# Kernel optimization log

Hardware: AMD Instinct MI355X
Metric: run time of the kernel (lower is better)

## Reference

```python
import jax, jax.numpy as jnp
import numpy as np

HEADS = 16

def _rope(x):
    # x: (B, H, T, D); rotate pairs (even, odd) along last dim, positions along axis 2
    B, H, T, D = x.shape
    half = D // 2
    theta = 10000.0 ** (-jnp.arange(half, dtype=x.dtype) / half)          # (half,)
    angles = jnp.arange(T, dtype=x.dtype)[:, None] * theta                # (T, half)
    sin, cos = jnp.sin(angles), jnp.cos(angles)                           # (T, half)
    x1, x2 = x[..., ::2], x[..., 1::2]                                    # (B,H,T,half)
    rot = jnp.stack([x1 * cos - x2 * sin, x1 * sin + x2 * cos], axis=-1)  # (B,H,T,half,2)
    return rot.reshape(B, H, T, D)

def setup_inputs() -> dict:
    key = jax.random.key(0)
    k1, k2, k3 = jax.random.split(key, 3)
    B, T, C = 2, 2048, 1024
    return {
        "x": jax.random.normal(k1, (B, T, C), dtype=jnp.float32),
        "W_qkv": jax.random.normal(k2, (3 * C, C), dtype=jnp.float32) * 0.02,
        "W_out": jax.random.normal(k3, (C, C), dtype=jnp.float32) * 0.02,
        "window": 256,
    }

def reference(x, W_qkv, W_out, window):
    B, T, C = x.shape
    H = HEADS
    D = C // H
    # fused QKV projection (torch Linear: y = x @ W.T)
    qkv = jnp.einsum('btc,fc->btf', x, W_qkv)            # (B,T,3C)
    qkv = qkv.reshape(B, T, H, 3 * D).transpose(0, 2, 1, 3)  # (B,H,T,3D)
    q, k, v = jnp.split(qkv, 3, axis=-1)                 # each (B,H,T,D)
    q, k = _rope(q), _rope(k)
    # causal + local-window boolean mask: allow j in [i-window, i]
    i = jnp.arange(T)[:, None]
    j = jnp.arange(T)[None, :]
    mask = (j <= i) & (j >= i - window)                  # (T,T) bool
    scale = 1.0 / jnp.sqrt(jnp.asarray(D, dtype=x.dtype))
    scores = jnp.einsum('bhqd,bhkd->bhqk', q, k) * scale # (B,H,T,T)
    scores = jnp.where(mask[None, None], scores, -jnp.inf)
    attn = jax.nn.softmax(scores, axis=-1)
    out = jnp.einsum('bhqk,bhkd->bhqd', attn, v)         # (B,H,T,D)
    out = out.transpose(0, 2, 1, 3).reshape(B, T, C)
    return jnp.einsum('btc,oc->bto', out, W_out)
```

## Files before the change

### kernel.cpp

```cpp
#include <hip/hip_runtime.h>

typedef float f32x4 __attribute__((ext_vector_type(4)));
typedef __bf16 bf16x8 __attribute__((ext_vector_type(8)));
typedef unsigned short u16x4 __attribute__((ext_vector_type(4)));

__device__ __forceinline__ unsigned short f2bf(float f) {
  union { float f; unsigned int u; } v; v.f = f;
  unsigned int r = (v.u + 0x7FFFu + ((v.u >> 16) & 1u)) >> 16;
  return (unsigned short)r;
}
__device__ __forceinline__ float bf2f(unsigned short h) {
  union { unsigned int u; float f; } v; v.u = ((unsigned int)h) << 16;
  return v.f;
}
__device__ __forceinline__ void gload_lds16(const void* g, void* l) {
  __builtin_amdgcn_global_load_lds(
      (const __attribute__((address_space(1))) unsigned int*)g,
      (__attribute__((address_space(3))) unsigned int*)l, 16, 0, 0);
}

__global__ __launch_bounds__(256) void prep_kernel(
    const float* __restrict__ x, const float* __restrict__ wqkv,
    const float* __restrict__ wout, unsigned short* __restrict__ xb,
    unsigned short* __restrict__ wqkvb, unsigned short* __restrict__ woutb,
    float2* __restrict__ tab) {
  const int N1 = 1048576, N2 = 786432, N3 = 262144;
  int idx = blockIdx.x * 256 + threadIdx.x;
  if (idx < N1 + N2 + N3) {
    const float* src; unsigned short* dst; int i = idx;
    if (i < N1)           { src = x;    dst = xb; }
    else if (i < N1 + N2) { i -= N1;      src = wqkv; dst = wqkvb; }
    else                  { i -= N1 + N2; src = wout; dst = woutb; }
    float4 v = ((const float4*)src)[i];
    u16x4 o;
    o.x = f2bf(v.x); o.y = f2bf(v.y); o.z = f2bf(v.z); o.w = f2bf(v.w);
    ((u16x4*)dst)[i] = o;
  } else {
    int i = idx - (N1 + N2 + N3);
    if (i < 65536) {
      int t = i >> 5, p = i & 31;
      float theta = exp2f(-(float)p * 0.4152410118609203f);
      float sn, cs;
      sincosf((float)t * theta, &sn, &cs);
      tab[i] = make_float2(cs, sn);
    }
  }
}

template <bool OUTBF16>
__global__ __launch_bounds__(256) void gemm_bt(const unsigned short* __restrict__ A,
                                               const unsigned short* __restrict__ B,
                                               void* __restrict__ C,
                                               int M, int N, int K) {
  __shared__ unsigned short As[128][32];
  __shared__ unsigned short Bs[128][32];
  const int tid = threadIdx.x;
  const int lane = tid & 63;
  const int w = tid >> 6, wr = w >> 1, wc = w & 1;
  const int bm = blockIdx.y * 128, bn = blockIdx.x * 128;
  const int t4 = tid >> 2, c8 = (tid & 3) * 8;
  const unsigned short* Ab = A + (size_t)(bm + t4) * K + c8;
  const unsigned short* Bb = B + (size_t)(bn + t4) * K + c8;
  const int rq = lane & 15, kg = (lane >> 4) * 8;
  f32x4 acc[4][4] = {};
  for (int kt = 0; kt < K; kt += 32) {
    gload_lds16(Ab + kt,                  &As[t4][c8]);
    gload_lds16(Ab + kt + (size_t)64 * K, &As[t4 + 64][c8]);
    gload_lds16(Bb + kt,                  &Bs[t4][c8]);
    gload_lds16(Bb + kt + (size_t)64 * K, &Bs[t4 + 64][c8]);
    __syncthreads();
    bf16x8 fa[4], fb[4];
#pragma unroll
    for (int m = 0; m < 4; ++m) fa[m] = *(const bf16x8*)&As[wr * 64 + m * 16 + rq][kg];
#pragma unroll
    for (int n = 0; n < 4; ++n) fb[n] = *(const bf16x8*)&Bs[wc * 64 + n * 16 + rq][kg];
#pragma unroll
    for (int m = 0; m < 4; ++m)
#pragma unroll
      for (int n = 0; n < 4; ++n)
        acc[m][n] = __builtin_amdgcn_mfma_f32_16x16x32_bf16(fa[m], fb[n], acc[m][n], 0, 0, 0);
    __syncthreads();
  }
  const int r0 = bm + wr * 64 + (lane >> 4) * 4;
  const int c0 = bn + wc * 64 + rq;
#pragma unroll
  for (int m = 0; m < 4; ++m)
#pragma unroll
    for (int n = 0; n < 4; ++n)
#pragma unroll
      for (int j = 0; j < 4; ++j) {
        int row = r0 + m * 16 + j, col = c0 + n * 16;
        if (OUTBF16)
          ((unsigned short*)C)[(size_t)row * N + col] = f2bf(acc[m][n][j]);
        else
          ((float*)C)[(size_t)row * N + col] = acc[m][n][j];
      }
}

#define WMAX 256

__device__ __forceinline__ void rope16(unsigned short* e, const float2* __restrict__ tb) {
#pragma unroll
  for (int p = 0; p < 8; ++p) {
    float2 cs = tb[p];
    float a = bf2f(e[2 * p]), b = bf2f(e[2 * p + 1]);
    e[2 * p]     = f2bf(a * cs.x - b * cs.y);
    e[2 * p + 1] = f2bf(a * cs.y + b * cs.x);
  }
}

__global__ __launch_bounds__(256) void attn_kernel(const unsigned short* __restrict__ qkv,
                                                   unsigned short* __restrict__ attnb,
                                                   const int* __restrict__ winp,
                                                   const float2* __restrict__ tab) {
  __shared__ unsigned short Qs[64][72];
  __shared__ unsigned short KPs[320 * 72];
  __shared__ unsigned short Vt[64][328];
  const int T = 2048;
  const int tid = threadIdx.x;
  const int bid = blockIdx.x;
  const int qt = bid & 31;
  const int bh = bid >> 5;
  const int b = bh >> 4, h = bh & 15;
  const int qbase = qt * 64;
  const int kbase = qbase - WMAX;
  const int win = *winp;
  const unsigned short* base = qkv + (size_t)b * T * 3072 + h * 192;
  const int tr = tid >> 2, tc = (tid & 3) * 16;
  const int vswz = (tid & 3) << 4;
  {
    const unsigned short* s = base + (size_t)(qbase + tr) * 3072 + tc;
    unsigned short tq[16];
    *(int4*)&tq[0] = *(const int4*)s;
    *(int4*)&tq[8] = *(const int4*)(s + 8);
    rope16(tq, tab + (qbase + tr) * 32 + tc / 2);
    *(int4*)&Qs[tr][tc]     = *(int4*)&tq[0];
    *(int4*)&Qs[tr][tc + 8] = *(int4*)&tq[8];
  }
#pragma unroll
  for (int p5 = 0; p5 < 5; ++p5) {
    int s = p5 * 64 + tr;
    int j = kbase + s;
    int jc = j < 0 ? 0 : j;
    const unsigned short* sk = base + (size_t)jc * 3072 + 64 + tc;
    unsigned short tk[16];
    *(int4*)&tk[0] = *(const int4*)sk;
    *(int4*)&tk[8] = *(const int4*)(sk + 8);
    rope16(tk, tab + jc * 32 + tc / 2);
    *(int4*)&KPs[s * 72 + tc]     = *(int4*)&tk[0];
    *(int4*)&KPs[s * 72 + tc + 8] = *(int4*)&tk[8];
    const unsigned short* sv = base + (size_t)jc * 3072 + 128 + tc;
    unsigned short tmp[16];
    *(int4*)&tmp[0] = *(const int4*)sv;
    *(int4*)&tmp[8] = *(const int4*)(sv + 8);
    int ssw = s ^ vswz;
#pragma unroll
    for (int e = 0; e < 16; ++e) Vt[tc + e][ssw] = tmp[e];
  }
  __syncthreads();
  const int lane = tid & 63, wv = tid >> 6;
  const int rbase = wv * 16;
  const int rq = lane & 15, kg = (lane >> 4) * 8;
  bf16x8 qa[2];
#pragma unroll
  for (int kk = 0; kk < 2; ++kk)
    qa[kk] = *(const bf16x8*)&Qs[rbase + rq][kk * 32 + kg];
  float sc[20][4];
#pragma unroll
  for (int n = 0; n < 20; ++n) {
    int jlo = kbase + n * 16;
    if (jlo + 15 >= 0 && jlo <= qbase + rbase + 15) {
      f32x4 s = {};
#pragma unroll
      for (int kk = 0; kk < 2; ++kk) {
        bf16x8 kb = *(const bf16x8*)&KPs[(n * 16 + rq) * 72 + kk * 32 + kg];
        s = __builtin_amdgcn_mfma_f32_16x16x32_bf16(qa[kk], kb, s, 0, 0, 0);
      }
#pragma unroll
      for (int r = 0; r < 4; ++r) sc[n][r] = s[r];
    } else {
#pragma unroll
      for (int r = 0; r < 4; ++r) sc[n][r] = -1e30f;
    }
  }
  const float scale = 0.125f;
#pragma unroll
  for (int r = 0; r < 4; ++r) {
    const int i = qbase + rbase + (lane >> 4) * 4 + r;
    float mx = -1e30f;
#pragma unroll
    for (int n = 0; n < 20; ++n) {
      int j = kbase + n * 16 + rq;
      bool valid = (j >= 0) && (j <= i) && (i - j <= win);
      float v = valid ? sc[n][r] * scale : -1e30f;
      sc[n][r] = v;
      mx = fmaxf(mx, v);
    }
#pragma unroll
    for (int off = 1; off < 16; off <<= 1) mx = fmaxf(mx, __shfl_xor(mx, off));
    float sum = 0.f;
#pragma unroll
    for (int n = 0; n < 20; ++n) {
      float pv = __expf(sc[n][r] - mx);
      sc[n][r] = pv;
      sum += pv;
    }
#pragma unroll
    for (int off = 1; off < 16; off <<= 1) sum += __shfl_xor(sum, off);
    float inv = 1.0f / sum;
#pragma unroll
    for (int n = 0; n < 20; ++n) sc[n][r] *= inv;
  }
  __syncthreads();
#pragma unroll
  for (int n = 0; n < 20; ++n)
#pragma unroll
    for (int r = 0; r < 4; ++r)
      KPs[(rbase + (lane >> 4) * 4 + r) * 328 + n * 16 + rq] = f2bf(sc[n][r]);
  f32x4 oacc[4] = {};
#pragma unroll
  for (int kk = 0; kk < 10; ++kk) {
    bf16x8 pa = *(const bf16x8*)&KPs[(rbase + rq) * 328 + kk * 32 + kg];
#pragma unroll
    for (int n = 0; n < 4; ++n) {
      bf16x8 vb = *(const bf16x8*)&Vt[n * 16 + rq][(kk * 32 + kg) ^ (n << 4)];
      oacc[n] = __builtin_amdgcn_mfma_f32_16x16x32_bf16(pa, vb, oacc[n], 0, 0, 0);
    }
  }
#pragma unroll
  for (int n = 0; n < 4; ++n)
#pragma unroll
    for (int j = 0; j < 4; ++j) {
      int r = qbase + rbase + (lane >> 4) * 4 + j;
      int d = n * 16 + rq;
      attnb[(size_t)(b * T + r) * 1024 + h * 64 + d] = f2bf(oacc[n][j]);
    }
}

extern "C" void kernel_launch(void* const* d_in, const int* in_sizes, int n_in,
                              void* d_out, int out_size, void* d_ws, size_t ws_size,
                              hipStream_t stream) {
  const float* x    = (const float*)d_in[0];
  const float* Wqkv = (const float*)d_in[1];
  const float* Wout = (const float*)d_in[2];
  const int*   winp = (const int*)d_in[3];

  const int M = 4096, C = 1024, N1 = 3072;
  unsigned short* xb    = (unsigned short*)d_ws;
  unsigned short* wqkvb = xb    + (size_t)M * C;
  unsigned short* woutb = wqkvb + (size_t)N1 * C;
  unsigned short* qkvb  = woutb + (size_t)C * C;
  unsigned short* attnb = qkvb  + (size_t)M * N1;
  float2*         tab   = (float2*)(attnb + (size_t)M * C);

  const int PREP = 1048576 + 786432 + 262144 + 65536;
  prep_kernel<<<(PREP + 255) / 256, 256, 0, stream>>>(x, Wqkv, Wout, xb, wqkvb,
                                                      woutb, tab);

  gemm_bt<true><<<dim3(N1 / 128, M / 128), 256, 0, stream>>>(xb, wqkvb, qkvb,
                                                             M, N1, C);

  attn_kernel<<<2 * 16 * 32, 256, 0, stream>>>(qkvb, attnb, winp, tab);

  gemm_bt<false><<<dim3(C / 128, M / 128), 256, 0, stream>>>(attnb, woutb,
                                                             (float*)d_out, M, C, C);
}
```

Before: 193.9 us.

## Split RoPE into separate pass and stream K into LDS with async loads

RoPE is moved out of the attention kernel into a separate in-place kernel over the QKV buffer. With pre-rotated data, the attention kernel loads Q straight into registers, fetches K with global_load_lds direct-to-LDS copies using an XOR swizzle, and reuses a single LDS buffer for K and P. LDS use drops, with launch bounds set for 2 blocks per SM. The extra kernel launch and one more read-write pass over Q/K add traffic, in exchange for removing redundant per-block RoPE work (each K row was rotated about five times) and raising occupancy.

Result: faster. 187.9 us (-3.1%).

```diff
diff --git a/kernel.cpp b/kernel.cpp
--- a/kernel.cpp
+++ b/kernel.cpp
@@ -97,25 +97,29 @@
       }
 }
 
+__global__ __launch_bounds__(256) void rope_inplace(unsigned short* __restrict__ qkv,
+                                                    const float2* __restrict__ tab) {
+  int idx = blockIdx.x * 256 + threadIdx.x;
+  int dp = idx & 31;
+  int t  = (idx >> 5) & 2047;
+  int bh = idx >> 16;
+  unsigned short* p = qkv + (size_t)((bh >> 4) * 2048 + t) * 3072 + (bh & 15) * 192 + dp * 2;
+  float2 cs = tab[t * 32 + dp];
+  float q1 = bf2f(p[0]), q2 = bf2f(p[1]);
+  p[0] = f2bf(q1 * cs.x - q2 * cs.y);
+  p[1] = f2bf(q1 * cs.y + q2 * cs.x);
+  float k1 = bf2f(p[64]), k2 = bf2f(p[65]);
+  p[64] = f2bf(k1 * cs.x - k2 * cs.y);
+  p[65] = f2bf(k1 * cs.y + k2 * cs.x);
+}
+
 #define WMAX 256
-
-__device__ __forceinline__ void rope16(unsigned short* e, const float2* __restrict__ tb) {
-#pragma unroll
-  for (int p = 0; p < 8; ++p) {
-    float2 cs = tb[p];
-    float a = bf2f(e[2 * p]), b = bf2f(e[2 * p + 1]);
-    e[2 * p]     = f2bf(a * cs.x - b * cs.y);
-    e[2 * p + 1] = f2bf(a * cs.y + b * cs.x);
-  }
-}
-
-__global__ __launch_bounds__(256) void attn_kernel(const unsigned short* __restrict__ qkv,
-                                                   unsigned short* __restrict__ attnb,
-                                                   const int* __restrict__ winp,
-                                                   const float2* __restrict__ tab) {
-  __shared__ unsigned short Qs[64][72];
-  __shared__ unsigned short KPs[320 * 72];
-  __shared__ unsigned short Vt[64][328];
+__global__ __launch_bounds__(256, 2) void attn_kernel(const unsigned short* __restrict__ qkv,
+                                                      unsigned short* __restrict__ attnb,
+                                                      const int* __restrict__ winp) {
+  __shared__ unsigned short lds[40960];
+  unsigned short* Ks = lds;
+  unsigned short* Vt = lds + 20480;
   const int T = 2048;
   const int tid = threadIdx.x;
   const int bid = blockIdx.x;
@@ -126,45 +130,45 @@
   const int kbase = qbase - WMAX;
   const int win = *winp;
   const unsigned short* base = qkv + (size_t)b * T * 3072 + h * 192;
-  const int tr = tid >> 2, tc = (tid & 3) * 16;
-  const int vswz = (tid & 3) << 4;
+  const int lane = tid & 63, wv = tid >> 6;
+  const int rq = lane & 15, hi = lane >> 4, kg = hi * 8;
+  const int rbase = wv * 16;
+  bf16x8 qa[2];
+#pragma unroll
+  for (int kk = 0; kk < 2; ++kk)
+    qa[kk] = *(const bf16x8*)(base + (size_t)(qbase + rbase + rq) * 3072 + kk * 32 + kg);
+#pragma unroll
+  for (int it = 0; it < 10; ++it) {
+    int ch = tid + it * 256;
+    int row = ch >> 3, blk = ch & 7;
+    int j = kbase + row;
+    int jc = j < 0 ? 0 : j;
+    gload_lds16(base + (size_t)jc * 3072 + 64 + ((blk ^ (row & 7)) * 8), Ks + ch * 8);
+  }
   {
-    const unsigned short* s = base + (size_t)(qbase + tr) * 3072 + tc;
-    unsigned short tq[16];
-    *(int4*)&tq[0] = *(const int4*)s;
-    *(int4*)&tq[8] = *(const int4*)(s + 8);
-    rope16(tq, tab + (qbase + tr) * 32 + tc / 2);
-    *(int4*)&Qs[tr][tc]     = *(int4*)&tq[0];
-    *(int4*)&Qs[tr][tc + 8] = *(int4*)&tq[8];
-  }
-#pragma unroll
-  for (int p5 = 0; p5 < 5; ++p5) {
-    int s = p5 * 64 + tr;
-    int j = kbase + s;
-    int jc = j < 0 ? 0 : j;
-    const unsigned short* sk = base + (size_t)jc * 3072 + 64 + tc;
-    unsigned short tk[16];
-    *(int4*)&tk[0] = *(const int4*)sk;
-    *(int4*)&tk[8] = *(const int4*)(sk + 8);
-    rope16(tk, tab + jc * 32 + tc / 2);
-    *(int4*)&KPs[s * 72 + tc]     = *(int4*)&tk[0];
-    *(int4*)&KPs[s * 72 + tc + 8] = *(int4*)&tk[8];
-    const unsigned short* sv = base + (size_t)jc * 3072 + 128 + tc;
-    unsigned short tmp[16];
-    *(int4*)&tmp[0] = *(const int4*)sv;
-    *(int4*)&tmp[8] = *(const int4*)(sv + 8);
-    int ssw = s ^ vswz;
-#pragma unroll
-    for (int e = 0; e < 16; ++e) Vt[tc + e][ssw] = tmp[e];
+    const int tr = tid >> 2, tc = (tid & 3) * 16;
+    const int vsw = tc;
+#pragma unroll
+    for (int p5 = 0; p5 < 5; ++p5) {
+      int s = p5 * 64 + tr;
+      int j = kbase + s;
+      int jc = j < 0 ? 0 : j;
+      const unsigned short* sv = base + (size_t)jc * 3072 + 128 + tc;
+      unsigned short tmp[16];
+      *(int4*)&tmp[0] = *(const int4*)sv;
+      *(int4*)&tmp[8] = *(const int4*)(sv + 8);
+      int scol = s ^ vsw;
+#pragma unroll
+      for (int e = 0; e < 16; ++e) {
+        int d = tc + e;
+        int col = scol + d * 8;
+        if (col >= 320) col -= 320;
+        if (col >= 320) col -= 320;
+        Vt[d * 320 + col] = tmp[e];
+      }
+    }
   }
   __syncthreads();
-  const int lane = tid & 63, wv = tid >> 6;
-  const int rbase = wv * 16;
-  const int rq = lane & 15, kg = (lane >> 4) * 8;
-  bf16x8 qa[2];
-#pragma unroll
-  for (int kk = 0; kk < 2; ++kk)
-    qa[kk] = *(const bf16x8*)&Qs[rbase + rq][kk * 32 + kg];
   float sc[20][4];
 #pragma unroll
   for (int n = 0; n < 20; ++n) {
@@ -173,7 +177,9 @@
       f32x4 s = {};
 #pragma unroll
       for (int kk = 0; kk < 2; ++kk) {
-        bf16x8 kb = *(const bf16x8*)&KPs[(n * 16 + rq) * 72 + kk * 32 + kg];
+        int row = n * 16 + rq;
+        int blk = (hi + kk * 4) ^ (row & 7);
+        bf16x8 kb = *(const bf16x8*)(Ks + row * 64 + blk * 8);
         s = __builtin_amdgcn_mfma_f32_16x16x32_bf16(qa[kk], kb, s, 0, 0, 0);
       }
 #pragma unroll
@@ -186,7 +192,7 @@
   const float scale = 0.125f;
 #pragma unroll
   for (int r = 0; r < 4; ++r) {
-    const int i = qbase + rbase + (lane >> 4) * 4 + r;
+    const int i = qbase + rbase + hi * 4 + r;
     float mx = -1e30f;
 #pragma unroll
     for (int n = 0; n < 20; ++n) {
@@ -215,15 +221,25 @@
 #pragma unroll
   for (int n = 0; n < 20; ++n)
 #pragma unroll
-    for (int r = 0; r < 4; ++r)
-      KPs[(rbase + (lane >> 4) * 4 + r) * 328 + n * 16 + rq] = f2bf(sc[n][r]);
+    for (int r = 0; r < 4; ++r) {
+      int q = rbase + hi * 4 + r;
+      int c = (n * 16 + rq) ^ ((q & 7) << 3);
+      Ks[q * 320 + c] = f2bf(sc[n][r]);
+    }
   f32x4 oacc[4] = {};
 #pragma unroll
   for (int kk = 0; kk < 10; ++kk) {
-    bf16x8 pa = *(const bf16x8*)&KPs[(rbase + rq) * 328 + kk * 32 + kg];
+    int prow = rbase + rq;
+    int pc = (kk * 32 + kg) ^ ((rq & 7) << 3);
+    bf16x8 pa = *(const bf16x8*)(Ks + prow * 320 + pc);
 #pragma unroll
     for (int n = 0; n < 4; ++n) {
-      bf16x8 vb = *(const bf16x8*)&Vt[n * 16 + rq][(kk * 32 + kg) ^ (n << 4)];
+      int d = n * 16 + rq;
+      int scol = (kk * 32 + kg) ^ ((n & 3) << 4);
+      int col = scol + d * 8;
+      if (col >= 320) col -= 320;
+      if (col >= 320) col -= 320;
+      bf16x8 vb = *(const bf16x8*)(Vt + d * 320 + col);
       oacc[n] = __builtin_amdgcn_mfma_f32_16x16x32_bf16(pa, vb, oacc[n], 0, 0, 0);
     }
   }
@@ -231,7 +247,7 @@
   for (int n = 0; n < 4; ++n)
 #pragma unroll
     for (int j = 0; j < 4; ++j) {
-      int r = qbase + rbase + (lane >> 4) * 4 + j;
+      int r = qbase + rbase + hi * 4 + j;
       int d = n * 16 + rq;
       attnb[(size_t)(b * T + r) * 1024 + h * 64 + d] = f2bf(oacc[n][j]);
     }
@@ -260,7 +276,9 @@
   gemm_bt<true><<<dim3(N1 / 128, M / 128), 256, 0, stream>>>(xb, wqkvb, qkvb,
                                                              M, N1, C);
 
-  attn_kernel<<<2 * 16 * 32, 256, 0, stream>>>(qkvb, attnb, winp, tab);
+  rope_inplace<<<(2 * 16 * 2048 * 32) / 256, 256, 0, stream>>>(qkvb, tab);
+
+  attn_kernel<<<2 * 16 * 32, 256, 0, stream>>>(qkvb, attnb, winp);
 
   gemm_bt<false><<<dim3(C / 128, M / 128), 256, 0, stream>>>(attnb, woutb,
                                                              (float*)d_out, M, C, C);
```
